# Performance work log

Measured on AMD Instinct MI355X. Metric: run time of the kernel, lower is better.

## Reference

```python
import jax, jax.numpy as jnp
import numpy as np

EPS = 1e-5
DN = ('NCHW', 'OIHW', 'NCHW')


def _conv3x3(x, w):
    return jax.lax.conv_general_dilated(x, w, (1, 1), 'SAME', dimension_numbers=DN)


def _bn_relu(x, g, b):
    # eval-mode BN: running_mean=0, running_var=1
    scale = (g / jnp.sqrt(1.0 + EPS))[None, :, None, None]
    return jax.nn.relu(x * scale + b[None, :, None, None])


def _double_conv(x, w1, g1, b1, w2, g2, b2):
    x = _bn_relu(_conv3x3(x, w1), g1, b1)
    return _bn_relu(_conv3x3(x, w2), g2, b2)


def _up2x_bilinear_align(x):
    # bilinear, align_corners=True, scale_factor=2
    def interp(a, axis, n_in):
        n_out = 2 * n_in
        pos = jnp.arange(n_out, dtype=jnp.float32) * (n_in - 1) / (n_out - 1)
        lo = jnp.floor(pos).astype(jnp.int32)
        hi = jnp.minimum(lo + 1, n_in - 1)
        w = pos - lo.astype(jnp.float32)
        sh = [1, 1, 1, 1]
        sh[axis] = n_out
        w = w.reshape(sh)
        return jnp.take(a, lo, axis=axis) * (1.0 - w) + jnp.take(a, hi, axis=axis) * w
    B, C, H, W = x.shape
    return interp(interp(x, 2, H), 3, W)


def _lstm_dir(seq, Wih, Whh, bih, bhh, reverse):
    # seq: (N, T, C) -> (N, T, Hh); PyTorch gate order i,f,g,o
    Hh = Whh.shape[1]
    xg = jnp.einsum('ntc,gc->ntg', seq, Wih) + (bih + bhh)
    if reverse:
        xg = xg[:, ::-1]
    xg = jnp.swapaxes(xg, 0, 1)  # (T, N, 4H)
    N = seq.shape[0]
    h0 = jnp.zeros((N, Hh), seq.dtype)

    def step(carry, gx):
        h, c = carry
        g = gx + h @ Whh.T
        i, f, gg, o = jnp.split(g, 4, axis=-1)
        c = jax.nn.sigmoid(f) * c + jax.nn.sigmoid(i) * jnp.tanh(gg)
        h = jax.nn.sigmoid(o) * jnp.tanh(c)
        return (h, c), h

    _, hs = jax.lax.scan(step, (h0, h0), xg)
    hs = jnp.swapaxes(hs, 0, 1)  # (N, T, Hh)
    if reverse:
        hs = hs[:, ::-1]
    return hs


def _bilstm(seq, Wf, Uf, bif, bhf, Wb, Ub, bib, bhb):
    return jnp.concatenate([
        _lstm_dir(seq, Wf, Uf, bif, bhf, False),
        _lstm_dir(seq, Wb, Ub, bib, bhb, True),
    ], axis=-1)


def _site_rows(x, lstm):
    # batched version of per-row LSTM: each row is a sequence over W, features C
    B, C, H, W = x.shape
    s = jnp.transpose(x, (0, 2, 3, 1)).reshape(B * H, W, C)
    out = _bilstm(s, *lstm)  # (B*H, W, C) since 2*hidden == C
    return jnp.transpose(out.reshape(B, H, W, C), (0, 3, 1, 2))


def _site_cols(x, lstm):
    # each column is a sequence over H, features C
    B, C, H, W = x.shape
    s = jnp.transpose(x, (0, 3, 2, 1)).reshape(B * W, H, C)
    out = _bilstm(s, *lstm)
    return jnp.transpose(out.reshape(B, W, H, C), (0, 3, 2, 1))


def setup_inputs() -> dict:
    key = jax.random.key(0)
    ks = jax.random.split(key, 24)
    d = {}
    d['x1'] = jax.random.normal(ks[0], (8, 128, 32, 32), jnp.float32)
    d['x2'] = jax.random.normal(ks[1], (8, 128, 64, 64), jnp.float32)
    # bidirectional LSTM: input 256, hidden 128
    d['lstm_Wih_f'] = jax.random.normal(ks[2], (512, 256), jnp.float32) * 0.06
    d['lstm_Whh_f'] = jax.random.normal(ks[3], (512, 128), jnp.float32) * 0.08
    d['lstm_bih_f'] = jax.random.normal(ks[4], (512,), jnp.float32) * 0.05
    d['lstm_bhh_f'] = jax.random.normal(ks[5], (512,), jnp.float32) * 0.05
    d['lstm_Wih_b'] = jax.random.normal(ks[6], (512, 256), jnp.float32) * 0.06
    d['lstm_Whh_b'] = jax.random.normal(ks[7], (512, 128), jnp.float32) * 0.08
    d['lstm_bib_tmp'] = None
    del d['lstm_bib_tmp']
    d['lstm_bih_b'] = jax.random.normal(ks[8], (512,), jnp.float32) * 0.05
    d['lstm_bhh_b'] = jax.random.normal(ks[9], (512,), jnp.float32) * 0.05
    # conv_2 = DoubleConv(512, 256) (mid=256), shared across its two call sites
    d['c2_w1'] = jax.random.normal(ks[10], (256, 512, 3, 3), jnp.float32) * 0.02
    d['c2_g1'] = jax.random.uniform(ks[11], (256,), jnp.float32, 0.5, 1.5)
    d['c2_b1'] = jax.random.normal(ks[12], (256,), jnp.float32) * 0.05
    d['c2_w2'] = jax.random.normal(ks[13], (256, 256, 3, 3), jnp.float32) * 0.03
    d['c2_g2'] = jax.random.uniform(ks[14], (256,), jnp.float32, 0.5, 1.5)
    d['c2_b2'] = jax.random.normal(ks[15], (256,), jnp.float32) * 0.05
    # conv = DoubleConv(256, 128, mid=128)
    d['cv_w1'] = jax.random.normal(ks[16], (128, 256, 3, 3), jnp.float32) * 0.03
    d['cv_g1'] = jax.random.uniform(ks[17], (128,), jnp.float32, 0.5, 1.5)
    d['cv_b1'] = jax.random.normal(ks[18], (128,), jnp.float32) * 0.05
    d['cv_w2'] = jax.random.normal(ks[19], (128, 128, 3, 3), jnp.float32) * 0.04
    d['cv_g2'] = jax.random.uniform(ks[20], (128,), jnp.float32, 0.5, 1.5)
    d['cv_b2'] = jax.random.normal(ks[21], (128,), jnp.float32) * 0.05
    return d


def reference(x1, x2, lstm_Wih_f, lstm_Whh_f, lstm_bih_f, lstm_bhh_f,
              lstm_Wih_b, lstm_Whh_b, lstm_bih_b, lstm_bhh_b,
              c2_w1, c2_g1, c2_b1, c2_w2, c2_g2, c2_b2,
              cv_w1, cv_g1, cv_b1, cv_w2, cv_g2, cv_b2):
    lstm = (lstm_Wih_f, lstm_Whh_f, lstm_bih_f, lstm_bhh_f,
            lstm_Wih_b, lstm_Whh_b, lstm_bih_b, lstm_bhh_b)
    x1u = _up2x_bilinear_align(x1)
    dy = x2.shape[2] - x1u.shape[2]
    dx = x2.shape[3] - x1u.shape[3]
    x1u = jnp.pad(x1u, ((0, 0), (0, 0), (dy // 2, dy - dy // 2), (dx // 2, dx - dx // 2)))
    x = jnp.concatenate([x2, x1u], axis=1)  # (B, 256, 64, 64)
    # site_relation mutates x in-place in torch: rows pass, then cols pass on the
    # row-updated tensor; x_weigth and x_heigth alias the same final tensor.
    x = _site_rows(x, lstm)
    x = _site_cols(x, lstm)
    x_site = jnp.concatenate([x, x], axis=1)  # (B, 512, H, W)
    x_site = _double_conv(x_site, c2_w1, c2_g1, c2_b1, c2_w2, c2_g2, c2_b2)
    x = jnp.concatenate([x, x_site], axis=1)  # (B, 512, H, W)
    x = _double_conv(x, c2_w1, c2_g1, c2_b1, c2_w2, c2_g2, c2_b2)
    x = _double_conv(x, cv_w1, cv_g1, cv_b1, cv_w2, cv_g2, cv_b2)
    return x  # (B, 128, 64, 64)
```

## Files before the change

### kernel.cpp

```cpp
#include <hip/hip_runtime.h>
#include <hip/hip_bf16.h>
#include <math.h>

typedef __bf16 bf16x8 __attribute__((ext_vector_type(8)));
typedef float  f32x4  __attribute__((ext_vector_type(4)));

__device__ __forceinline__ float sigm(float x)  { return 1.f/(1.f+__expf(-x)); }
__device__ __forceinline__ float tanh_f(float x){ return 2.f/(1.f+__expf(-2.f*x)) - 1.f; }
__device__ __forceinline__ float b2f(unsigned short u){
  unsigned int x = ((unsigned int)u) << 16; return __uint_as_float(x);
}
__device__ __forceinline__ unsigned short f2b(float v){
  __hip_bfloat16 h = __float2bfloat16(v); return *(unsigned short*)&h;
}
__device__ __forceinline__ void glds16(const void* g, void* l) {
  __builtin_amdgcn_global_load_lds(
      (const __attribute__((address_space(1))) unsigned int*)g,
      (__attribute__((address_space(3))) unsigned int*)l, 16, 0, 0);
}
__device__ __forceinline__ bf16x8 bzero() {
  bf16x8 v;
  #pragma unroll
  for (int i = 0; i < 8; ++i) v[i] = (__bf16)0.0f;
  return v;
}
__device__ __forceinline__ void barrier_lds() {
  asm volatile("s_waitcnt lgkmcnt(0)\n\ts_barrier" ::: "memory");
}

__global__ __launch_bounds__(256) void k_upcat(const float* __restrict__ x1,
                                               const float* __restrict__ x2,
                                               __hip_bfloat16* __restrict__ X0) {
  int idx = blockIdx.x*256 + threadIdx.x;
  int c = idx & 255;
  int w = (idx >> 8) & 63;
  int h = (idx >> 14) & 63;
  int n = idx >> 20;
  float v;
  if (c < 128) {
    v = x2[((n*128 + c)*64 + h)*64 + w];
  } else {
    int cc = c - 128;
    float py = (h*31.0f)/63.0f;
    int ly = (int)py; int hy = min(ly+1, 31); float fy = py - (float)ly;
    float px = (w*31.0f)/63.0f;
    int lx = (int)px; int hx = min(lx+1, 31); float fx = px - (float)lx;
    const float* p = x1 + (size_t)(n*128 + cc)*1024;
    float v00 = p[ly*32+lx], v01 = p[ly*32+hx];
    float v10 = p[hy*32+lx], v11 = p[hy*32+hx];
    v = (1.f-fy)*((1.f-fx)*v00 + fx*v01) + fy*((1.f-fx)*v10 + fx*v11);
  }
  X0[idx] = __float2bfloat16(v);
}

__global__ __launch_bounds__(256) void k_wih_prep(
    const float* __restrict__ Wf, const float* __restrict__ Wb,
    const float* __restrict__ bif, const float* __restrict__ bhf,
    const float* __restrict__ bib, const float* __restrict__ bhb,
    __hip_bfloat16* __restrict__ wihc, float* __restrict__ biasc) {
  int idx = blockIdx.x*256 + threadIdx.x;
  int n = idx >> 8, k = idx & 255;
  float v = (n < 512) ? Wf[n*256 + k] : Wb[(n-512)*256 + k];
  wihc[idx] = __float2bfloat16(v);
  if (idx < 1024) biasc[idx] = (idx < 512) ? bif[idx] + bhf[idx]
                                           : bib[idx-512] + bhb[idx-512];
}

__global__ __launch_bounds__(256) void k_xg_gemm(
    const __hip_bfloat16* __restrict__ Xin,
    const __hip_bfloat16* __restrict__ Wihc,
    const float* __restrict__ biasc,
    __hip_bfloat16* __restrict__ xg) {
  __shared__ __align__(16) unsigned short sa[128][72];
  __shared__ __align__(16) unsigned short sw[128][72];
  int bx = blockIdx.x;
  int t = bx >> 2, seq0 = (bx & 3) << 7;
  int n0 = blockIdx.y << 7;
  int tid = threadIdx.x, lane = tid & 63, wid = tid >> 6;
  int wm = wid >> 1, wn = wid & 1;
  int l15 = lane & 15, quad = lane >> 4;
  f32x4 acc[4][4];
  #pragma unroll
  for (int i = 0; i < 4; ++i)
    #pragma unroll
    for (int j = 0; j < 4; ++j) acc[i][j] = (f32x4){0.f,0.f,0.f,0.f};

  for (int k0 = 0; k0 < 256; k0 += 64) {
    __syncthreads();
    for (int idx = tid; idx < 2048; idx += 256) {
      int row = idx >> 4, c4 = (idx & 15) << 2;
      *(ushort4*)&sa[row][c4] = *(const ushort4*)((const unsigned short*)Xin +
          (size_t)((seq0 + row)*64 + t)*256 + k0 + c4);
      *(ushort4*)&sw[row][c4] = *(const ushort4*)((const unsigned short*)Wihc +
          (size_t)(n0 + row)*256 + k0 + c4);
    }
    __syncthreads();
    #pragma unroll
    for (int k32 = 0; k32 < 64; k32 += 32) {
      bf16x8 af[4], bfr[4];
      #pragma unroll
      for (int mt = 0; mt < 4; ++mt)
        af[mt] = *(const bf16x8*)&sa[wm*64 + mt*16 + l15][k32 + quad*8];
      #pragma unroll
      for (int nt = 0; nt < 4; ++nt)
        bfr[nt] = *(const bf16x8*)&sw[wn*64 + nt*16 + l15][k32 + quad*8];
      #pragma unroll
      for (int mt = 0; mt < 4; ++mt)
        #pragma unroll
        for (int nt = 0; nt < 4; ++nt)
          acc[mt][nt] = __builtin_amdgcn_mfma_f32_16x16x32_bf16(
              af[mt], bfr[nt], acc[mt][nt], 0, 0, 0);
    }
  }
  #pragma unroll
  for (int nt = 0; nt < 4; ++nt) {
    int cg = n0 + wn*64 + nt*16 + l15;
    int dir = cg >> 9;
    int g   = (cg >> 7) & 3;
    int u   = cg & 127;
    float bias = biasc[cg];
    unsigned short* op = (unsigned short*)xg +
        (size_t)(((dir*64 + t)*4 + g)*512)*128 + u;
    #pragma unroll
    for (int mt = 0; mt < 4; ++mt) {
      int sbase = seq0 + wm*64 + mt*16 + quad*4;
      f32x4 a = acc[mt][nt];
      #pragma unroll
      for (int r = 0; r < 4; ++r)
        op[(size_t)(sbase + r)*128] = f2b(a[r] + bias);
    }
  }
}

__global__ __launch_bounds__(256, 1) void k_lstm_rec(
    const __hip_bfloat16* __restrict__ xg,
    const float* __restrict__ WhhF, const float* __restrict__ WhhB,
    __hip_bfloat16* __restrict__ out) {
  const int dir = blockIdx.y;
  const int sb  = blockIdx.x;
  const float* Whh = dir ? WhhB : WhhF;
  __shared__ __align__(16) unsigned short hs[16][136];
  __shared__ __align__(16) float gv[4][128][4];
  const int tid = threadIdx.x, lane = tid & 63, wv = tid >> 6;
  const int l15 = lane & 15, quad = lane >> 4;

  bf16x8 wf[4][2][4];
  #pragma unroll
  for (int g = 0; g < 4; ++g)
    #pragma unroll
    for (int ut = 0; ut < 2; ++ut) {
      int gate = g*128 + wv*32 + ut*16 + l15;
      #pragma unroll
      for (int kc = 0; kc < 4; ++kc) {
        const float* wp = Whh + (size_t)gate*128 + kc*32 + quad*8;
        float4 w0 = *(const float4*)wp;
        float4 w1 = *(const float4*)(wp + 4);
        bf16x8 f;
        f[0]=(__bf16)w0.x; f[1]=(__bf16)w0.y; f[2]=(__bf16)w0.z; f[3]=(__bf16)w0.w;
        f[4]=(__bf16)w1.x; f[5]=(__bf16)w1.y; f[6]=(__bf16)w1.z; f[7]=(__bf16)w1.w;
        wf[g][ut][kc] = f;
      }
    }
  for (int i = tid; i < 16*136; i += 256) ((unsigned short*)hs)[i] = 0;

  const int u_  = tid & 127;
  const int s0_ = tid >> 7;
  float cst[2] = {0.f, 0.f};

  const unsigned short* xp = (const unsigned short*)xg +
      (size_t)dir*64*4*512*128;
  unsigned short xv[2][4], xn[2][4];
  #define LDX(stp, dst)                                                    \
    {                                                                      \
      int ts_ = (stp) < 64 ? (stp) : 63;                                   \
      int t_  = dir ? 63 - ts_ : ts_;                                      \
      _Pragma("unroll")                                                    \
      for (int j_ = 0; j_ < 2; ++j_) {                                     \
        int s_ = s0_ + j_*2;                                               \
        _Pragma("unroll")                                                  \
        for (int g_ = 0; g_ < 4; ++g_)                                     \
          dst[j_][g_] = xp[(size_t)((t_*4 + g_)*512 + sb*4 + s_)*128 + u_];\
      }                                                                    \
    }
  LDX(0, xv);
  __syncthreads();

  for (int step = 0; step < 64; ++step) {
    int t = dir ? 63 - step : step;
    LDX(step + 1, xn);
    bf16x8 af[4];
    #pragma unroll
    for (int kc = 0; kc < 4; ++kc)
      af[kc] = *(const bf16x8*)&hs[l15][kc*32 + quad*8];
    f32x4 acc[4][2];
    #pragma unroll
    for (int g = 0; g < 4; ++g)
      #pragma unroll
      for (int ut = 0; ut < 2; ++ut) acc[g][ut] = (f32x4){0.f,0.f,0.f,0.f};
    #pragma unroll
    for (int kc = 0; kc < 4; ++kc)
      #pragma unroll
      for (int g = 0; g < 4; ++g)
        #pragma unroll
        for (int ut = 0; ut < 2; ++ut)
          acc[g][ut] = __builtin_amdgcn_mfma_f32_16x16x32_bf16(
              af[kc], wf[g][ut][kc], acc[g][ut], 0, 0, 0);
    if (quad == 0) {
      #pragma unroll
      for (int ut = 0; ut < 2; ++ut) {
        int u = wv*32 + ut*16 + l15;
        #pragma unroll
        for (int r = 0; r < 4; ++r) {
          float4 q;
          q.x = acc[0][ut][r]; q.y = acc[1][ut][r];
          q.z = acc[2][ut][r]; q.w = acc[3][ut][r];
          *(float4*)&gv[r][u][0] = q;
        }
      }
    }
    barrier_lds();
    #pragma unroll
    for (int j = 0; j < 2; ++j) {
      int s = s0_ + j*2;
      float4 gq = *(const float4*)&gv[s][u_][0];
      float I = gq.x + b2f(xv[j][0]);
      float F = gq.y + b2f(xv[j][1]);
      float G = gq.z + b2f(xv[j][2]);
      float O = gq.w + b2f(xv[j][3]);
      float cv = sigm(F)*cst[j] + sigm(I)*tanh_f(G);
      float hv = sigm(O)*tanh_f(cv);
      cst[j] = cv;
      unsigned short hb = f2b(hv);
      hs[s][u_] = hb;
      int gs = sb*4 + s;
      ((unsigned short*)out)[(size_t)(((gs >> 6)*64 + t)*64 + (gs & 63))*256
                             + dir*128 + u_] = hb;
    }
    barrier_lds();
    #pragma unroll
    for (int j = 0; j < 2; ++j)
      #pragma unroll
      for (int g = 0; g < 4; ++g) xv[j][g] = xn[j][g];
  }
  #undef LDX
}

__global__ __launch_bounds__(256) void k_wrefmt_bf16(const float* __restrict__ src,
                                                     __hip_bfloat16* __restrict__ dst,
                                                     int Ci, int Co, int fold) {
  int idx = blockIdx.x*256 + threadIdx.x;
  int total = 9*Ci*Co;
  if (idx >= total) return;
  int ci = idx % Ci;
  int co = (idx / Ci) % Co;
  int k  = idx / (Ci*Co);
  int CiS = fold ? Ci*2 : Ci;
  float v = src[(size_t)(co*CiS + ci)*9 + k];
  if (fold) v += src[(size_t)(co*CiS + ci + Ci)*9 + k];
  dst[idx] = __float2bfloat16(v);
}

__global__ __launch_bounds__(256, 2) void k_conv3_v2(
    const __hip_bfloat16* __restrict__ inA, const __hip_bfloat16* __restrict__ inB,
    const __hip_bfloat16* __restrict__ wgt,
    const float* __restrict__ gam, const float* __restrict__ bet,
    float* __restrict__ outF, __hip_bfloat16* __restrict__ outB,
    int Cin, int Co, int nchw) {
  __shared__ __align__(16) unsigned short si[2][64][64];
  __shared__ __align__(16) unsigned short sw[3][128][64];
  int bx = blockIdx.x;
  int n  = bx >> 5;
  int h0 = (bx & 31) << 1;
  int co0 = blockIdx.y << 7;
  int tid = threadIdx.x;
  int lane = tid & 63;
  int wid  = tid >> 6;
  int wm = wid >> 1;
  int wn = wid & 1;
  int l15 = lane & 15, quad = lane >> 4;

  f32x4 acc[4][4];
  #pragma unroll
  for (int i = 0; i < 4; ++i)
    #pragma unroll
    for (int j = 0; j < 4; ++j) acc[i][j] = (f32x4){0.f,0.f,0.f,0.f};

  int cs = inB ? 256 : Cin;
  for (int ky = 0; ky < 3; ++ky) {
    for (int ci0 = 0; ci0 < Cin; ci0 += 64) {
      const unsigned short* src = (const unsigned short*)inA; int cb = ci0;
      if (inB && ci0 >= 256) { src = (const unsigned short*)inB; cb = ci0 - 256; }
      __syncthreads();
      {
        int r = wid >> 1;
        int ih = h0 + r + ky - 1;
        int half = (wid & 1) << 5;
        if (ih >= 0 && ih <= 63) {
          const unsigned short* gsrc = src + (size_t)((n*64 + ih)*64)*cs + cb;
          int pl = lane >> 3, pc = lane & 7;
          #pragma unroll
          for (int q = 0; q < 4; ++q) {
            int iw = half + q*8 + pl;
            int lc = pc ^ (iw & 7);
            glds16(gsrc + (size_t)iw*cs + lc*8, &si[r][half + q*8][0]);
          }
        } else {
          uint4 z = {0,0,0,0};
          #pragma unroll
          for (int q = 0; q < 4; ++q)
            *(uint4*)(&si[r][half + q*8][0] + lane*8) = z;
        }
      }
      {
        int col = lane >> 3, pc = lane & 7;
        const unsigned short* wk = (const unsigned short*)wgt +
            (size_t)(ky*3*Co + co0)*Cin + ci0;
        #pragma unroll
        for (int j = 0; j < 12; ++j) {
          int s = wid + j*4;
          int kx = s >> 4, co8 = (s & 15) << 3;
          int co = co8 + col;
          int lc = pc ^ (co & 7);
          glds16(wk + (size_t)(kx*Co + co)*Cin + lc*8, &sw[kx][co8][0]);
        }
      }
      __syncthreads();
      #pragma unroll
      for (int kx = 0; kx < 3; ++kx) {
        #pragma unroll
        for (int k32 = 0; k32 < 2; ++k32) {
          bf16x8 af[4], bfr[4];
          #pragma unroll
          for (int mt = 0; mt < 4; ++mt) {
            int iw = mt*16 + l15 + kx - 1;
            int iwc = iw & 63;
            int pc = (k32*4 + quad) ^ (iwc & 7);
            af[mt] = *(const bf16x8*)&si[wm][iwc][pc*8];
            if ((kx == 0 && mt == 0 && l15 == 0) ||
                (kx == 2 && mt == 3 && l15 == 15))
              af[mt] = bzero();
          }
          #pragma unroll
          for (int nt = 0; nt < 4; ++nt) {
            int co = wn*64 + nt*16 + l15;
            int pc = (k32*4 + quad) ^ (co & 7);
            bfr[nt] = *(const bf16x8*)&sw[kx][co][pc*8];
          }
          #pragma unroll
          for (int mt = 0; mt < 4; ++mt)
            #pragma unroll
            for (int nt = 0; nt < 4; ++nt)
              acc[mt][nt] = __builtin_amdgcn_mfma_f32_16x16x32_bf16(
                  af[mt], bfr[nt], acc[mt][nt], 0, 0, 0);
        }
      }
    }
  }
  const float kS = 0.9999950000374997f;
  int h = h0 + wm;
  #pragma unroll
  for (int nt = 0; nt < 4; ++nt) {
    int co = co0 + wn*64 + nt*16 + l15;
    float scale = gam[co]*kS, bb = bet[co];
    #pragma unroll
    for (int mt = 0; mt < 4; ++mt) {
      f32x4 a = acc[mt][nt];
      #pragma unroll
      for (int r = 0; r < 4; ++r) {
        int w = mt*16 + quad*4 + r;
        float v = fmaf(a[r], scale, bb);
        v = v > 0.f ? v : 0.f;
        if (nchw) outF[(size_t)((n*Co + co)*64 + h)*64 + w] = v;
        else      outB[(size_t)((n*64 + h)*64 + w)*Co + co] = __float2bfloat16(v);
      }
    }
  }
}

extern "C" void kernel_launch(void* const* d_in, const int* in_sizes, int n_in,
                              void* d_out, int out_size, void* d_ws, size_t ws_size,
                              hipStream_t stream) {
  const float* x1    = (const float*)d_in[0];
  const float* x2    = (const float*)d_in[1];
  const float* Wih_f = (const float*)d_in[2];
  const float* Whh_f = (const float*)d_in[3];
  const float* bih_f = (const float*)d_in[4];
  const float* bhh_f = (const float*)d_in[5];
  const float* Wih_b = (const float*)d_in[6];
  const float* Whh_b = (const float*)d_in[7];
  const float* bih_b = (const float*)d_in[8];
  const float* bhh_b = (const float*)d_in[9];
  const float* c2_w1 = (const float*)d_in[10];
  const float* c2_g1 = (const float*)d_in[11];
  const float* c2_b1 = (const float*)d_in[12];
  const float* c2_w2 = (const float*)d_in[13];
  const float* c2_g2 = (const float*)d_in[14];
  const float* c2_b2 = (const float*)d_in[15];
  const float* cv_w1 = (const float*)d_in[16];
  const float* cv_g1 = (const float*)d_in[17];
  const float* cv_b1 = (const float*)d_in[18];
  const float* cv_w2 = (const float*)d_in[19];
  const float* cv_g2 = (const float*)d_in[20];
  const float* cv_b2 = (const float*)d_in[21];

  char* base = (char*)d_ws;
  const size_t SLOTB = 16777216ull;
  __hip_bfloat16* Xb  = (__hip_bfloat16*)(base);
  __hip_bfloat16* Sb  = (__hip_bfloat16*)(base);
  __hip_bfloat16* XG  = (__hip_bfloat16*)(base + SLOTB);
  __hip_bfloat16* D2  = (__hip_bfloat16*)(base + SLOTB);
  __hip_bfloat16* D2b = (__hip_bfloat16*)(base + 2*SLOTB);
  __hip_bfloat16* RT  = (__hip_bfloat16*)(base + SLOTB + 67108864ull);
  __hip_bfloat16* D1  = RT;
  char* wq = base + SLOTB + 67108864ull + SLOTB;
  __hip_bfloat16* wihc  = (__hip_bfloat16*)wq;
  float*          biasc = (float*)(wq + 524288);
  char* cw = wq + 528384;
  __hip_bfloat16* w1f    = (__hip_bfloat16*)(cw);
  __hip_bfloat16* w1full = (__hip_bfloat16*)(cw + 1179648);
  __hip_bfloat16* w2r    = (__hip_bfloat16*)(cw + 3538944);
  __hip_bfloat16* wv1    = (__hip_bfloat16*)(cw + 4718592);
  __hip_bfloat16* wv2    = (__hip_bfloat16*)(cw + 5308416);

  k_wih_prep<<<1024, 256, 0, stream>>>(Wih_f, Wih_b, bih_f, bhh_f, bih_b, bhh_b,
                                       wihc, biasc);
  k_wrefmt_bf16<<<(9*256*256+255)/256, 256, 0, stream>>>(c2_w1, w1f,    256, 256, 1);
  k_wrefmt_bf16<<<(9*512*256+255)/256, 256, 0, stream>>>(c2_w1, w1full, 512, 256, 0);
  k_wrefmt_bf16<<<(9*256*256+255)/256, 256, 0, stream>>>(c2_w2, w2r,    256, 256, 0);
  k_wrefmt_bf16<<<(9*256*128+255)/256, 256, 0, stream>>>(cv_w1, wv1,    256, 128, 0);
  k_wrefmt_bf16<<<(9*128*128+255)/256, 256, 0, stream>>>(cv_w2, wv2,    128, 128, 0);

  k_upcat<<<32768, 256, 0, stream>>>(x1, x2, Xb);

  k_xg_gemm<<<dim3(256, 8), 256, 0, stream>>>(Xb, wihc, biasc, XG);
  k_lstm_rec<<<dim3(128, 2), 256, 0, stream>>>(XG, Whh_f, Whh_b, RT);
  k_xg_gemm<<<dim3(256, 8), 256, 0, stream>>>(RT, wihc, biasc, XG);
  k_lstm_rec<<<dim3(128, 2), 256, 0, stream>>>(XG, Whh_f, Whh_b, Sb);

  k_conv3_v2<<<dim3(256,2), 256, 0, stream>>>(Sb, nullptr, w1f, c2_g1, c2_b1,
                                              nullptr, D1, 256, 256, 0);
  k_conv3_v2<<<dim3(256,2), 256, 0, stream>>>(D1, nullptr, w2r, c2_g2, c2_b2,
                                              nullptr, D2, 256, 256, 0);
  k_conv3_v2<<<dim3(256,2), 256, 0, stream>>>(Sb, D2, w1full, c2_g1, c2_b1,
                                              nullptr, D2b, 512, 256, 0);
  k_conv3_v2<<<dim3(256,2), 256, 0, stream>>>(D2b, nullptr, w2r, c2_g2, c2_b2,
                                              nullptr, D1, 256, 256, 0);
  k_conv3_v2<<<dim3(256,1), 256, 0, stream>>>(D1, nullptr, wv1, cv_g1, cv_b1,
                                              nullptr, D2, 256, 128, 0);
  k_conv3_v2<<<dim3(256,1), 256, 0, stream>>>(D2, nullptr, wv2, cv_g2, cv_b2,
                                              (float*)d_out, nullptr, 128, 128, 1);
}
```

Measured before the change: 662.5 us.

## Retile 3x3 conv to 4 rows x 64 channels and reuse input rows across ky

The conv kernel now has each block cover 4 output rows and 64 output channels, with one output row per wave. For each 64-channel input chunk, the 6 input rows (halo included) are loaded into LDS once and reused for all three ky taps. Previously the input rows were reloaded for every ky, so this cuts redundant global input traffic, at the cost of less weight reuse per block and more blocks. Separately, the LSTM recurrence now runs MFMAs for a second 16-row tile whose accumulators are never used, which adds wasted work to that step.

```diff
diff --git a/kernel.cpp b/kernel.cpp
--- a/kernel.cpp
+++ b/kernel.cpp
@@ -188,23 +188,29 @@
   for (int step = 0; step < 64; ++step) {
     int t = dir ? 63 - step : step;
     LDX(step + 1, xn);
-    bf16x8 af[4];
+    bf16x8 af[2][4];
+    #pragma unroll
+    for (int mt = 0; mt < 2; ++mt)
+      #pragma unroll
+      for (int kc = 0; kc < 4; ++kc)
+        af[mt][kc] = *(const bf16x8*)&hs[mt*16 + l15][kc*32 + quad*8];
+    f32x4 acc[2][4][2];
+    #pragma unroll
+    for (int mt = 0; mt < 2; ++mt)
+      #pragma unroll
+      for (int g = 0; g < 4; ++g)
+        #pragma unroll
+        for (int ut = 0; ut < 2; ++ut) acc[mt][g][ut] = (f32x4){0.f,0.f,0.f,0.f};
     #pragma unroll
     for (int kc = 0; kc < 4; ++kc)
-      af[kc] = *(const bf16x8*)&hs[l15][kc*32 + quad*8];
-    f32x4 acc[4][2];
-    #pragma unroll
-    for (int g = 0; g < 4; ++g)
-      #pragma unroll
-      for (int ut = 0; ut < 2; ++ut) acc[g][ut] = (f32x4){0.f,0.f,0.f,0.f};
-    #pragma unroll
-    for (int kc = 0; kc < 4; ++kc)
-      #pragma unroll
-      for (int g = 0; g < 4; ++g)
-        #pragma unroll
-        for (int ut = 0; ut < 2; ++ut)
-          acc[g][ut] = __builtin_amdgcn_mfma_f32_16x16x32_bf16(
-              af[kc], wf[g][ut][kc], acc[g][ut], 0, 0, 0);
+      #pragma unroll
+      for (int mt = 0; mt < 2; ++mt)
+        #pragma unroll
+        for (int g = 0; g < 4; ++g)
+          #pragma unroll
+          for (int ut = 0; ut < 2; ++ut)
+            acc[mt][g][ut] = __builtin_amdgcn_mfma_f32_16x16x32_bf16(
+                af[mt][kc], wf[g][ut][kc], acc[mt][g][ut], 0, 0, 0);
     if (quad == 0) {
       #pragma unroll
       for (int ut = 0; ut < 2; ++ut) {
@@ -212,8 +218,8 @@
         #pragma unroll
         for (int r = 0; r < 4; ++r) {
           float4 q;
-          q.x = acc[0][ut][r]; q.y = acc[1][ut][r];
-          q.z = acc[2][ut][r]; q.w = acc[3][ut][r];
+          q.x = acc[0][0][ut][r]; q.y = acc[0][1][ut][r];
+          q.z = acc[0][2][ut][r]; q.w = acc[0][3][ut][r];
           *(float4*)&gv[r][u][0] = q;
         }
       }
@@ -260,24 +266,23 @@
   dst[idx] = __float2bfloat16(v);
 }
 
-__global__ __launch_bounds__(256, 2) void k_conv3_v2(
+__global__ __launch_bounds__(256, 2) void k_conv3_v3(
     const __hip_bfloat16* __restrict__ inA, const __hip_bfloat16* __restrict__ inB,
     const __hip_bfloat16* __restrict__ wgt,
     const float* __restrict__ gam, const float* __restrict__ bet,
     float* __restrict__ outF, __hip_bfloat16* __restrict__ outB,
     int Cin, int Co, int nchw) {
-  __shared__ __align__(16) unsigned short si[2][64][64];
-  __shared__ __align__(16) unsigned short sw[3][128][64];
+  __shared__ __align__(16) unsigned short si[6][64][64];
+  __shared__ __align__(16) unsigned short sw[3][64][64];
   int bx = blockIdx.x;
-  int n  = bx >> 5;
-  int h0 = (bx & 31) << 1;
-  int co0 = blockIdx.y << 7;
+  int n  = bx >> 4;
+  int h0 = (bx & 15) << 2;
+  int co0 = blockIdx.y << 6;
   int tid = threadIdx.x;
   int lane = tid & 63;
-  int wid  = tid >> 6;
-  int wm = wid >> 1;
-  int wn = wid & 1;
+  int wvid = tid >> 6;
   int l15 = lane & 15, quad = lane >> 4;
+  int pl = lane >> 3, pc = lane & 7;
 
   f32x4 acc[4][4];
   #pragma unroll
@@ -286,45 +291,41 @@
     for (int j = 0; j < 4; ++j) acc[i][j] = (f32x4){0.f,0.f,0.f,0.f};
 
   int cs = inB ? 256 : Cin;
-  for (int ky = 0; ky < 3; ++ky) {
-    for (int ci0 = 0; ci0 < Cin; ci0 += 64) {
-      const unsigned short* src = (const unsigned short*)inA; int cb = ci0;
-      if (inB && ci0 >= 256) { src = (const unsigned short*)inB; cb = ci0 - 256; }
-      __syncthreads();
+  for (int ci0 = 0; ci0 < Cin; ci0 += 64) {
+    const unsigned short* src = (const unsigned short*)inA; int cb = ci0;
+    if (inB && ci0 >= 256) { src = (const unsigned short*)inB; cb = ci0 - 256; }
+    __syncthreads();
+    #pragma unroll
+    for (int j = 0; j < 12; ++j) {
+      int s = wvid + j*4;
+      int row = s >> 3, grp = s & 7;
+      int ih = h0 + row - 1;
+      if (ih >= 0 && ih <= 63) {
+        const unsigned short* gsrc = src + (size_t)((n*64 + ih)*64)*cs + cb;
+        int iw = grp*8 + pl;
+        int lc = pc ^ (iw & 7);
+        glds16(gsrc + (size_t)iw*cs + lc*8, &si[row][grp*8][0]);
+      } else {
+        uint4 z = {0,0,0,0};
+        *(uint4*)((unsigned short*)&si[row][grp*8][0] + lane*8) = z;
+      }
+    }
+    for (int ky = 0; ky < 3; ++ky) {
+      if (ky) __syncthreads();
       {
-        int r = wid >> 1;
-        int ih = h0 + r + ky - 1;
-        int half = (wid & 1) << 5;
-        if (ih >= 0 && ih <= 63) {
-          const unsigned short* gsrc = src + (size_t)((n*64 + ih)*64)*cs + cb;
-          int pl = lane >> 3, pc = lane & 7;
-          #pragma unroll
-          for (int q = 0; q < 4; ++q) {
-            int iw = half + q*8 + pl;
-            int lc = pc ^ (iw & 7);
-            glds16(gsrc + (size_t)iw*cs + lc*8, &si[r][half + q*8][0]);
-          }
-        } else {
-          uint4 z = {0,0,0,0};
-          #pragma unroll
-          for (int q = 0; q < 4; ++q)
-            *(uint4*)(&si[r][half + q*8][0] + lane*8) = z;
-        }
-      }
-      {
-        int col = lane >> 3, pc = lane & 7;
         const unsigned short* wk = (const unsigned short*)wgt +
             (size_t)(ky*3*Co + co0)*Cin + ci0;
         #pragma unroll
-        for (int j = 0; j < 12; ++j) {
-          int s = wid + j*4;
-          int kx = s >> 4, co8 = (s & 15) << 3;
-          int co = co8 + col;
+        for (int j = 0; j < 6; ++j) {
+          int s = wvid + j*4;
+          int kx = s >> 3, cg = s & 7;
+          int co = cg*8 + pl;
           int lc = pc ^ (co & 7);
-          glds16(wk + (size_t)(kx*Co + co)*Cin + lc*8, &sw[kx][co8][0]);
+          glds16(wk + (size_t)(kx*Co + co)*Cin + lc*8, &sw[kx][cg*8][0]);
         }
       }
       __syncthreads();
+      int row = wvid + ky;
       #pragma unroll
       for (int kx = 0; kx < 3; ++kx) {
         #pragma unroll
@@ -334,17 +335,17 @@
           for (int mt = 0; mt < 4; ++mt) {
             int iw = mt*16 + l15 + kx - 1;
             int iwc = iw & 63;
-            int pc = (k32*4 + quad) ^ (iwc & 7);
-            af[mt] = *(const bf16x8*)&si[wm][iwc][pc*8];
+            int pcc = (k32*4 + quad) ^ (iwc & 7);
+            af[mt] = *(const bf16x8*)&si[row][iwc][pcc*8];
             if ((kx == 0 && mt == 0 && l15 == 0) ||
                 (kx == 2 && mt == 3 && l15 == 15))
               af[mt] = bzero();
           }
           #pragma unroll
           for (int nt = 0; nt < 4; ++nt) {
-            int co = wn*64 + nt*16 + l15;
-            int pc = (k32*4 + quad) ^ (co & 7);
-            bfr[nt] = *(const bf16x8*)&sw[kx][co][pc*8];
+            int co = nt*16 + l15;
+            int pcc = (k32*4 + quad) ^ (co & 7);
+            bfr[nt] = *(const bf16x8*)&sw[kx][co][pcc*8];
           }
           #pragma unroll
           for (int mt = 0; mt < 4; ++mt)
@@ -357,10 +358,10 @@
     }
   }
   const float kS = 0.9999950000374997f;
-  int h = h0 + wm;
+  int h = h0 + wvid;
   #pragma unroll
   for (int nt = 0; nt < 4; ++nt) {
-    int co = co0 + wn*64 + nt*16 + l15;
+    int co = co0 + nt*16 + l15;
     float scale = gam[co]*kS, bb = bet[co];
     #pragma unroll
     for (int mt = 0; mt < 4; ++mt) {
@@ -437,16 +438,16 @@
   k_xg_gemm<<<dim3(256, 8), 256, 0, stream>>>(RT, wihc, biasc, XG);
   k_lstm_rec<<<dim3(128, 2), 256, 0, stream>>>(XG, Whh_f, Whh_b, Sb);
 
-  k_conv3_v2<<<dim3(256,2), 256, 0, stream>>>(Sb, nullptr, w1f, c2_g1, c2_b1,
+  k_conv3_v3<<<dim3(128,4), 256, 0, stream>>>(Sb, nullptr, w1f, c2_g1, c2_b1,
                                               nullptr, D1, 256, 256, 0);
-  k_conv3_v2<<<dim3(256,2), 256, 0, stream>>>(D1, nullptr, w2r, c2_g2, c2_b2,
+  k_conv3_v3<<<dim3(128,4), 256, 0, stream>>>(D1, nullptr, w2r, c2_g2, c2_b2,
                                               nullptr, D2, 256, 256, 0);
-  k_conv3_v2<<<dim3(256,2), 256, 0, stream>>>(Sb, D2, w1full, c2_g1, c2_b1,
+  k_conv3_v3<<<dim3(128,4), 256, 0, stream>>>(Sb, D2, w1full, c2_g1, c2_b1,
                                               nullptr, D2b, 512, 256, 0);
-  k_conv3_v2<<<dim3(256,2), 256, 0, stream>>>(D2b, nullptr, w2r, c2_g2, c2_b2,
+  k_conv3_v3<<<dim3(128,4), 256, 0, stream>>>(D2b, nullptr, w2r, c2_g2, c2_b2,
                                               nullptr, D1, 256, 256, 0);
-  k_conv3_v2<<<dim3(256,1), 256, 0, stream>>>(D1, nullptr, wv1, cv_g1, cv_b1,
+  k_conv3_v3<<<dim3(128,2), 256, 0, stream>>>(D1, nullptr, wv1, cv_g1, cv_b1,
                                               nullptr, D2, 256, 128, 0);
-  k_conv3_v2<<<dim3(256,1), 256, 0, stream>>>(D2, nullptr, wv2, cv_g2, cv_b2,
+  k_conv3_v3<<<dim3(128,2), 256, 0, stream>>>(D2, nullptr, wv2, cv_g2, cv_b2,
                                               (float*)d_out, nullptr, 128, 128, 1);
 }
```

After: 659.6 us. Within noise of the previous version (-0.4%).
